# Performance work log

Measured on AMD Instinct MI355X. Metric: run time of the kernel, lower is better.

The kernel has to match this reference:

```python
import jax, jax.numpy as jnp
import numpy as np

BIGNET_DIM = 1024
GROUP_SIZE = 16
N_TOKENS = 65536
N_LINEARS = 12  # 4 blocks x 3 Linear4Bit
N_BLOCKS = 4
LN_EPS = 1e-5


def setup_inputs() -> dict:
    key = jax.random.key(0)
    k_x, k_q, k_s, k_b = jax.random.split(key, 4)
    D, G = BIGNET_DIM, BIGNET_DIM // GROUP_SIZE
    x = jax.random.normal(k_x, (N_TOKENS, D), dtype=jnp.float32)
    # int4 codes in [-8, 7], stored as int8; one scale per group of 16 input channels per output row
    qw = jax.random.randint(k_q, (N_LINEARS, D, D), -8, 8, dtype=jnp.int8)
    scales = jax.random.uniform(k_s, (N_LINEARS, D, G), dtype=jnp.float32, minval=0.005, maxval=0.02)
    bias = jax.random.normal(k_b, (N_LINEARS, D), dtype=jnp.float32) * 0.01
    ln_w = jnp.ones((N_BLOCKS, D), dtype=jnp.float32)
    ln_b = jnp.zeros((N_BLOCKS, D), dtype=jnp.float32)
    return {"x": x, "qw": qw, "scales": scales, "bias": bias, "ln_w": ln_w, "ln_b": ln_b}


def reference(x, qw, scales, bias, ln_w, ln_b):
    D = x.shape[-1]

    def lin4bit(h, i):
        # group-wise dequant: w[o, g*gs + j] = q[o, g*gs + j] * scale[o, g]
        w = (qw[i].astype(jnp.float32).reshape(D, -1, GROUP_SIZE) * scales[i][:, :, None]).reshape(D, D)
        return h @ w.T + bias[i]

    def layernorm(h, j):
        mu = jnp.mean(h, axis=-1, keepdims=True)
        var = jnp.mean(jnp.square(h - mu), axis=-1, keepdims=True)
        return (h - mu) / jnp.sqrt(var + LN_EPS) * ln_w[j] + ln_b[j]

    h = x
    for blk in range(N_BLOCKS):
        r = h
        h = jax.nn.relu(lin4bit(h, 3 * blk + 0))
        h = jax.nn.relu(lin4bit(h, 3 * blk + 1))
        h = lin4bit(h, 3 * blk + 2) + r
        h = layernorm(h, blk)
    return h
```

## Files before the change

### kernel.cpp

```cpp
#include <hip/hip_runtime.h>
#include <cstdint>
#include <cstddef>

typedef _Float16 h16;
typedef __attribute__((ext_vector_type(8))) _Float16 half8;
typedef __attribute__((ext_vector_type(4))) _Float16 half4;
typedef __attribute__((ext_vector_type(4))) float f32x4;

#define D 1024
#define NTOK 65536
#define BM 128
#define BN 128
#define BK 64
#define KTILES (D / BK)
#define NLIN 12

__device__ __forceinline__ size_t swz_pos(int t, int o) {
  return (size_t)t * D + ((o >> 6) << 6) + ((((o >> 3) & 7) ^ (t & 7)) << 3) + (o & 7);
}

__global__ __launch_bounds__(256) void k_dequant(const int* __restrict__ q,
                                                 const float* __restrict__ s,
                                                 h16* __restrict__ W) {
  const int row = blockIdx.x;
  const int o = row & (D - 1);
  const int k0 = threadIdx.x * 4;
  const int4 qv = *(const int4*)(q + (size_t)row * D + k0);
  const float sc = s[(size_t)row * (D / 16) + (k0 >> 4)];
  half4 wv;
  wv.x = (h16)((float)qv.x * sc);
  wv.y = (h16)((float)qv.y * sc);
  wv.z = (h16)((float)qv.z * sc);
  wv.w = (h16)((float)qv.w * sc);
  const int chunk = k0 >> 6;
  const int pg = (k0 >> 3) & 7;
  const size_t idx = (size_t)row * D + (chunk << 6) + (((pg ^ (o & 7)) << 3) + (k0 & 7));
  *(half4*)(W + idx) = wv;
}

__global__ __launch_bounds__(256) void k_convert(const float* __restrict__ x, h16* __restrict__ X) {
  const int idx = blockIdx.x * 256 + threadIdx.x;
  const int t = idx >> 7, g = idx & 127;
  const int tk = ((g >> 3) << 6) + (((g & 7) ^ (t & 7)) << 3);
  const float* src = x + (size_t)t * D + tk;
  const f32x4 a = *(const f32x4*)(src);
  const f32x4 b = *(const f32x4*)(src + 4);
  half8 v;
  v[0] = (h16)a.x; v[1] = (h16)a.y; v[2] = (h16)a.z; v[3] = (h16)a.w;
  v[4] = (h16)b.x; v[5] = (h16)b.y; v[6] = (h16)b.z; v[7] = (h16)b.w;
  *(half8*)(X + (size_t)t * D + (size_t)g * 8) = v;
}

__global__ __launch_bounds__(256, 4) void k_gemm(const h16* __restrict__ A,
                                                 const h16* __restrict__ W,
                                                 const float* __restrict__ bias,
                                                 const h16* res, h16* out, int relu) {
  __shared__ _Float16 lds_s[BM * BK * 2];
  _Float16* ldsA = lds_s;
  _Float16* ldsB = lds_s + BM * BK;

  const int bid = blockIdx.x;
  const int swzb = (bid & 7) * 512 + (bid >> 3);
  const int tm = swzb >> 3;
  const int tn = swzb & 7;
  const int tid = threadIdx.x;
  const int lane = tid & 63;
  const int w = tid >> 6;
  const int wm = w >> 1, wn = w & 1;

  int aoff[4][2], boff[4][2];
#pragma unroll
  for (int f = 0; f < 4; ++f) {
#pragma unroll
    for (int h = 0; h < 2; ++h) {
      const int ra = wm * 64 + f * 16 + (lane & 15);
      const int pa = (h * 4 + (lane >> 4)) ^ (ra & 7);
      aoff[f][h] = ra * BK + pa * 8;
      const int rb = wn * 64 + f * 16 + (lane & 15);
      const int pb = (h * 4 + (lane >> 4)) ^ (rb & 7);
      boff[f][h] = rb * BK + pb * 8;
    }
  }

  const h16* asrc[4];
  const h16* bsrc[4];
#pragma unroll
  for (int it = 0; it < 4; ++it) {
    const int gidx = w * 256 + it * 64 + lane;
    const int row = gidx >> 3, p = gidx & 7;
    asrc[it] = A + (size_t)(tm * BM + row) * D + p * 8;
    bsrc[it] = W + (size_t)(tn * BN + row) * D + p * 8;
  }

  f32x4 acc[4][4];
#pragma unroll
  for (int i = 0; i < 4; ++i)
#pragma unroll
    for (int j = 0; j < 4; ++j) acc[i][j] = (f32x4)0.f;

  for (int kt = 0; kt < KTILES; ++kt) {
    {
      _Float16* la = ldsA + w * 2048;
      _Float16* lb = ldsB + w * 2048;
#pragma unroll
      for (int it = 0; it < 4; ++it) {
        __builtin_amdgcn_global_load_lds(
            (const __attribute__((address_space(1))) void*)(asrc[it] + (size_t)kt * BK),
            (__attribute__((address_space(3))) void*)(la + it * 512), 16, 0, 0);
        __builtin_amdgcn_global_load_lds(
            (const __attribute__((address_space(1))) void*)(bsrc[it] + (size_t)kt * BK),
            (__attribute__((address_space(3))) void*)(lb + it * 512), 16, 0, 0);
      }
    }
    __syncthreads();

    half8 af[4][2], bf[4][2];
#pragma unroll
    for (int f = 0; f < 4; ++f) {
#pragma unroll
      for (int h = 0; h < 2; ++h) {
        af[f][h] = *(const half8*)(&ldsA[aoff[f][h]]);
        bf[f][h] = *(const half8*)(&ldsB[boff[f][h]]);
      }
    }
#pragma unroll
    for (int h = 0; h < 2; ++h)
#pragma unroll
      for (int mf = 0; mf < 4; ++mf)
#pragma unroll
        for (int nf = 0; nf < 4; ++nf)
          acc[mf][nf] = __builtin_amdgcn_mfma_f32_16x16x32_f16(af[mf][h], bf[nf][h], acc[mf][nf], 0, 0, 0);

    __syncthreads();
  }

  _Float16* ldc = lds_s;
#pragma unroll
  for (int nf = 0; nf < 4; ++nf) {
    const int ol = wn * 64 + nf * 16 + (lane & 15);
    const float bv = bias[tn * BN + ol];
#pragma unroll
    for (int mf = 0; mf < 4; ++mf) {
      const int tl0 = wm * 64 + mf * 16 + ((lane >> 4) << 2);
#pragma unroll
      for (int j = 0; j < 4; ++j) {
        const int tl = tl0 + j;
        float v = acc[mf][nf][j] + bv;
        if (relu) v = fmaxf(v, 0.f);
        ldc[tl * 128 + ((ol >> 6) << 6) + ((((ol >> 3) & 7) ^ (tl & 7)) << 3) + (ol & 7)] = (h16)v;
      }
    }
  }
  __syncthreads();

#pragma unroll
  for (int p = 0; p < 8; ++p) {
    const int g = p * 256 + tid;
    const int tl = g >> 4, c = g & 15;
    half8 v = *(const half8*)(ldc + tl * 128 + c * 8);
    const size_t gpos = (size_t)(tm * BM + tl) * D + tn * BN + c * 8;
    if (res) {
      const half8 r = *(const half8*)(res + gpos);
#pragma unroll
      for (int j = 0; j < 8; ++j) v[j] = (h16)((float)v[j] + (float)r[j]);
    }
    *(half8*)(out + gpos) = v;
  }
}

__device__ __forceinline__ void ln_stats(const half8& v0, const half8& v1, float& mu, float& rs) {
  float sum = 0.f, ss = 0.f;
#pragma unroll
  for (int j = 0; j < 8; ++j) {
    float f0 = (float)v0[j], f1 = (float)v1[j];
    sum += f0 + f1;
    ss += f0 * f0 + f1 * f1;
  }
#pragma unroll
  for (int m = 32; m > 0; m >>= 1) {
    sum += __shfl_xor(sum, m);
    ss += __shfl_xor(ss, m);
  }
  mu = sum * (1.f / D);
  const float var = ss * (1.f / D) - mu * mu;
  rs = rsqrtf(var + 1e-5f);
}

__global__ __launch_bounds__(256) void k_ln_mid(h16* h, const float* __restrict__ w, const float* __restrict__ b) {
  const int t = blockIdx.x * 4 + (threadIdx.x >> 6);
  const int lane = threadIdx.x & 63;
  h16* row = h + (size_t)t * D;
  half8 v0 = *(const half8*)(row + (size_t)lane * 8);
  half8 v1 = *(const half8*)(row + (size_t)(lane + 64) * 8);
  float mu, rs;
  ln_stats(v0, v1, mu, rs);
  const int tk0 = ((lane >> 3) << 6) + (((lane & 7) ^ (t & 7)) << 3);
  const int g1 = lane + 64;
  const int tk1 = ((g1 >> 3) << 6) + (((g1 & 7) ^ (t & 7)) << 3);
#pragma unroll
  for (int j = 0; j < 8; ++j) {
    v0[j] = (h16)(((float)v0[j] - mu) * rs * w[tk0 + j] + b[tk0 + j]);
    v1[j] = (h16)(((float)v1[j] - mu) * rs * w[tk1 + j] + b[tk1 + j]);
  }
  *(half8*)(row + (size_t)lane * 8) = v0;
  *(half8*)(row + (size_t)(lane + 64) * 8) = v1;
}

__global__ __launch_bounds__(256) void k_ln_final(const h16* __restrict__ h, const float* __restrict__ w,
                                                  const float* __restrict__ b, float* __restrict__ out) {
  const int t = blockIdx.x * 4 + (threadIdx.x >> 6);
  const int lane = threadIdx.x & 63;
  const h16* row = h + (size_t)t * D;
  half8 v0 = *(const half8*)(row + (size_t)lane * 8);
  half8 v1 = *(const half8*)(row + (size_t)(lane + 64) * 8);
  float mu, rs;
  ln_stats(v0, v1, mu, rs);
  const int tk0 = ((lane >> 3) << 6) + (((lane & 7) ^ (t & 7)) << 3);
  const int g1 = lane + 64;
  const int tk1 = ((g1 >> 3) << 6) + (((g1 & 7) ^ (t & 7)) << 3);
  float* orow = out + (size_t)t * D;
#pragma unroll
  for (int j = 0; j < 8; ++j) {
    orow[tk0 + j] = ((float)v0[j] - mu) * rs * w[tk0 + j] + b[tk0 + j];
    orow[tk1 + j] = ((float)v1[j] - mu) * rs * w[tk1 + j] + b[tk1 + j];
  }
}

extern "C" void kernel_launch(void* const* d_in, const int* in_sizes, int n_in,
                              void* d_out, int out_size, void* d_ws, size_t ws_size,
                              hipStream_t stream) {
  const float* x = (const float*)d_in[0];
  const int* qw = (const int*)d_in[1];
  const float* scales = (const float*)d_in[2];
  const float* bias = (const float*)d_in[3];
  const float* lnw = (const float*)d_in[4];
  const float* lnb = (const float*)d_in[5];
  float* out = (float*)d_out;

  if (ws_size < (size_t)152 * 1024 * 1024) return;

  char* ws = (char*)d_ws;
  h16* X = (h16*)ws;
  h16* W = (h16*)(ws + (size_t)128 * 1024 * 1024);
  h16* Y = (h16*)d_out;
  h16* Z = Y + (size_t)64 * 1024 * 1024;

  k_dequant<<<NLIN * D, 256, 0, stream>>>(qw, scales, W);
  k_convert<<<(NTOK * (D / 8)) / 256, 256, 0, stream>>>(x, X);

  const int GG = (NTOK / BM) * (D / BN);
  for (int blk = 0; blk < 4; ++blk) {
    const int l0 = 3 * blk;
    k_gemm<<<GG, 256, 0, stream>>>(X, W + (size_t)(l0 + 0) * D * D, bias + (l0 + 0) * D, nullptr, Y, 1);
    k_gemm<<<GG, 256, 0, stream>>>(Y, W + (size_t)(l0 + 1) * D * D, bias + (l0 + 1) * D, nullptr, Z, 1);
    k_gemm<<<GG, 256, 0, stream>>>(Z, W + (size_t)(l0 + 2) * D * D, bias + (l0 + 2) * D, X, X, 0);
    if (blk < 3)
      k_ln_mid<<<NTOK / 4, 256, 0, stream>>>(X, lnw + blk * D, lnb + blk * D);
    else
      k_ln_final<<<NTOK / 4, 256, 0, stream>>>(X, lnw + blk * D, lnb + blk * D, out);
  }
}
```

Before: 2.444 ms.

## Double-buffer LDS tiles in GEMM to overlap global loads with MFMA

The GEMM main loop now uses two LDS buffers for the A and B tiles. It issues the next tile's global-to-LDS loads before computing on the current tile, and uses explicit vmcnt waits and barriers to order the two. MFMA priority is raised with s_setprio while the MFMAs issue. This doubles LDS use to 64KB per block, so launch bounds drop from 4 to 2 blocks per CU, trading occupancy for latency hiding.

After: 2.623 ms. 1.07x slower.

```diff
diff --git a/kernel.cpp b/kernel.cpp
--- a/kernel.cpp
+++ b/kernel.cpp
@@ -14,6 +14,7 @@
 #define BK 64
 #define KTILES (D / BK)
 #define NLIN 12
+#define TILE_HALFS (BM * BK)
 
 __device__ __forceinline__ size_t swz_pos(int t, int o) {
   return (size_t)t * D + ((o >> 6) << 6) + ((((o >> 3) & 7) ^ (t & 7)) << 3) + (o & 7);
@@ -51,13 +52,11 @@
   *(half8*)(X + (size_t)t * D + (size_t)g * 8) = v;
 }
 
-__global__ __launch_bounds__(256, 4) void k_gemm(const h16* __restrict__ A,
+__global__ __launch_bounds__(256, 2) void k_gemm(const h16* __restrict__ A,
                                                  const h16* __restrict__ W,
                                                  const float* __restrict__ bias,
                                                  const h16* res, h16* out, int relu) {
-  __shared__ _Float16 lds_s[BM * BK * 2];
-  _Float16* ldsA = lds_s;
-  _Float16* ldsB = lds_s + BM * BK;
+  __shared__ _Float16 lds_s[4 * TILE_HALFS];
 
   const int bid = blockIdx.x;
   const int swzb = (bid & 7) * 512 + (bid >> 3);
@@ -98,21 +97,36 @@
 #pragma unroll
     for (int j = 0; j < 4; ++j) acc[i][j] = (f32x4)0.f;
 
+  auto stage = [&](int buf, int kt) {
+    _Float16* la = lds_s + buf * (2 * TILE_HALFS) + w * 2048;
+    _Float16* lb = la + TILE_HALFS;
+#pragma unroll
+    for (int it = 0; it < 4; ++it) {
+      __builtin_amdgcn_global_load_lds(
+          (const __attribute__((address_space(1))) void*)(asrc[it] + (size_t)kt * BK),
+          (__attribute__((address_space(3))) void*)(la + it * 512), 16, 0, 0);
+      __builtin_amdgcn_global_load_lds(
+          (const __attribute__((address_space(1))) void*)(bsrc[it] + (size_t)kt * BK),
+          (__attribute__((address_space(3))) void*)(lb + it * 512), 16, 0, 0);
+    }
+  };
+
+  stage(0, 0);
+
   for (int kt = 0; kt < KTILES; ++kt) {
-    {
-      _Float16* la = ldsA + w * 2048;
-      _Float16* lb = ldsB + w * 2048;
-#pragma unroll
-      for (int it = 0; it < 4; ++it) {
-        __builtin_amdgcn_global_load_lds(
-            (const __attribute__((address_space(1))) void*)(asrc[it] + (size_t)kt * BK),
-            (__attribute__((address_space(3))) void*)(la + it * 512), 16, 0, 0);
-        __builtin_amdgcn_global_load_lds(
-            (const __attribute__((address_space(1))) void*)(bsrc[it] + (size_t)kt * BK),
-            (__attribute__((address_space(3))) void*)(lb + it * 512), 16, 0, 0);
-      }
-    }
-    __syncthreads();
+    const int cur = kt & 1;
+    const _Float16* ldsA = lds_s + cur * (2 * TILE_HALFS);
+    const _Float16* ldsB = ldsA + TILE_HALFS;
+
+    if (kt + 1 < KTILES) {
+      stage(cur ^ 1, kt + 1);
+      asm volatile("s_waitcnt vmcnt(8)" ::: "memory");
+    } else {
+      asm volatile("s_waitcnt vmcnt(0)" ::: "memory");
+    }
+    __builtin_amdgcn_sched_barrier(0);
+    __builtin_amdgcn_s_barrier();
+    __builtin_amdgcn_sched_barrier(0);
 
     half8 af[4][2], bf[4][2];
 #pragma unroll
@@ -123,6 +137,10 @@
         bf[f][h] = *(const half8*)(&ldsB[boff[f][h]]);
       }
     }
+    asm volatile("s_waitcnt lgkmcnt(0)" ::: "memory");
+    __builtin_amdgcn_sched_barrier(0);
+
+    __builtin_amdgcn_s_setprio(1);
 #pragma unroll
     for (int h = 0; h < 2; ++h)
 #pragma unroll
@@ -130,8 +148,9 @@
 #pragma unroll
         for (int nf = 0; nf < 4; ++nf)
           acc[mf][nf] = __builtin_amdgcn_mfma_f32_16x16x32_f16(af[mf][h], bf[nf][h], acc[mf][nf], 0, 0, 0);
-
-    __syncthreads();
+    __builtin_amdgcn_s_setprio(0);
+    __builtin_amdgcn_sched_barrier(0);
+    __builtin_amdgcn_s_barrier();
   }
 
   _Float16* ldc = lds_s;
```
